# Kernel optimization log

Measured on AMD Instinct MI355X. Metric: run time of the kernel, lower is better.

The kernel has to match this reference:

```python
import jax, jax.numpy as jnp
import numpy as np

HEADS = 8


def setup_inputs() -> dict:
    key = jax.random.key(0)
    ks = jax.random.split(key, 6)
    B, N, D = 4, 2048, 512
    return {
        "x": jax.random.normal(ks[0], (B, N, D), dtype=jnp.float32),
        "pos": jax.random.uniform(ks[1], (B, N, 3), dtype=jnp.float32),
        "qkv_w": jax.random.normal(ks[2], (3 * D, D), dtype=jnp.float32) * 0.02,
        "qkv_b": jax.random.normal(ks[3], (3 * D,), dtype=jnp.float32) * 0.02,
        "out_w": jax.random.normal(ks[4], (D, D), dtype=jnp.float32) * 0.02,
        "out_b": jax.random.normal(ks[5], (D,), dtype=jnp.float32) * 0.02,
    }


def reference(x, pos, qkv_w, qkv_b, out_w, out_b):
    B, N, D = x.shape
    H = HEADS
    Dh = D // H
    scale = D ** (-0.5)  # NOTE: original uses full dim, not head dim

    # QKV projection -> [3, B, H, N, Dh]
    qkv = (x @ qkv_w.T + qkv_b).reshape(B, N, 3, H, Dh).transpose(2, 0, 3, 1, 4)
    q, k, v = qkv[0], qkv[1], qkv[2]

    # partial 3D RoPE on first 6 head dims (3 axis pairs)
    theta = pos * jnp.pi                    # [B, N, 3]
    sin = jnp.sin(theta)[:, None]           # [B, 1, N, 3] broadcasts over heads
    cos = jnp.cos(theta)[:, None]

    def rotate(t):
        x_rot = t[..., :6]
        x1 = x_rot[..., 0::2]               # [B, H, N, 3]
        x2 = x_rot[..., 1::2]
        return jnp.concatenate(
            [x1 * cos - x2 * sin, x1 * sin + x2 * cos, t[..., 6:]], axis=-1
        )

    q = rotate(q)
    k = rotate(k)

    attn = jax.nn.softmax(jnp.einsum("bhqd,bhkd->bhqk", q, k) * scale, axis=-1)
    out = jnp.einsum("bhqk,bhkd->bhqd", attn, v)          # [B, H, N, Dh]
    out = out.transpose(0, 2, 1, 3).reshape(B, N, D)
    return out @ out_w.T + out_b
```

## Files before the change

### kernel.cpp

```cpp
#include <hip/hip_runtime.h>
#include <stdint.h>

typedef __attribute__((ext_vector_type(4))) float f32x4;
typedef __attribute__((ext_vector_type(16))) float f32x16;
typedef __attribute__((ext_vector_type(8))) short bf16x8;
typedef __attribute__((ext_vector_type(4))) unsigned short u16x4;

__device__ __forceinline__ unsigned short f2bf(float f) {
    unsigned int u = __builtin_bit_cast(unsigned int, f);
    u += 0x7fffu + ((u >> 16) & 1u);
    return (unsigned short)(u >> 16);
}
__device__ __forceinline__ float bf2f(unsigned short s) {
    unsigned int u = ((unsigned int)s) << 16;
    return __builtin_bit_cast(float, u);
}
__device__ __forceinline__ float fexp2(float x) {
#if __has_builtin(__builtin_amdgcn_exp2f)
    return __builtin_amdgcn_exp2f(x);
#else
    return exp2f(x);
#endif
}
__device__ __forceinline__ unsigned int cvt_pk_bf16(float lo, float hi) {
    unsigned int r;
    asm("v_cvt_pk_bf16_f32 %0, %1, %2" : "=v"(r) : "v"(lo), "v"(hi));
    return r;
}

__global__ void k_cvt3(const float* __restrict__ x,
                       const float* __restrict__ w1,
                       const float* __restrict__ w2,
                       unsigned short* __restrict__ out) {
    const int C1 = 1048576;
    const int C2 = 196608;
    int i = blockIdx.x * blockDim.x + threadIdx.x;
    f32x4 v;
    if (i < C1)            v = ((const f32x4*)x)[i];
    else if (i < C1 + C2)  v = ((const f32x4*)w1)[i - C1];
    else                   v = ((const f32x4*)w2)[i - C1 - C2];
    u16x4 o;
    o.x = f2bf(v.x); o.y = f2bf(v.y); o.z = f2bf(v.z); o.w = f2bf(v.w);
    ((u16x4*)out)[i] = o;
}

__global__ __launch_bounds__(256, 3)
void k_gemm_qkv(const unsigned short* __restrict__ A,
                const unsigned short* __restrict__ Bm,
                const float* __restrict__ bias,
                const float* __restrict__ pos,
                unsigned short* __restrict__ Qb,
                unsigned short* __restrict__ Kb,
                unsigned short* __restrict__ VT) {
    const float PI = 3.14159265358979323846f;
    const float QS = 0.04419417382415922f * 1.44269504088896341f;
    const int K = 512;
    __shared__ unsigned short As[3][128 * 32];
    __shared__ unsigned short Bs[3][128 * 32];
    const int tid = threadIdx.x;
    const int lane = tid & 63;
    const int w = tid >> 6;
    const int wr = (w >> 1) * 64, wc = (w & 1) * 64;
    const int g = lane >> 4, fr = lane & 15;

    const int bid = blockIdx.x;
    const int xcd = bid & 7, loc = bid >> 3;
    const int rowb = xcd * 8 + (loc & 7);
    const int colb = loc >> 3;

    f32x4 acc[4][4];
#pragma unroll
    for (int i = 0; i < 4; ++i)
#pragma unroll
        for (int j = 0; j < 4; ++j) acc[i][j] = f32x4{0.f, 0.f, 0.f, 0.f};

    const int srow16 = lane >> 2;
    const int schunk = ((lane & 3) ^ (srow16 & 3)) * 8;
    const int sA = w, sB = w + 4;
    const unsigned short* Aseg0 = A + (size_t)(rowb * 128 + sA * 16 + srow16) * K + schunk;
    const unsigned short* Aseg1 = A + (size_t)(rowb * 128 + sB * 16 + srow16) * K + schunk;
    const unsigned short* Bseg0 = Bm + (size_t)(colb * 128 + sA * 16 + srow16) * K + schunk;
    const unsigned short* Bseg1 = Bm + (size_t)(colb * 128 + sB * 16 + srow16) * K + schunk;

    auto stage = [&](int bsel, int k0) {
        char* la = (char*)&As[bsel][0];
        char* lb = (char*)&Bs[bsel][0];
        __builtin_amdgcn_global_load_lds((const __attribute__((address_space(1))) void*)(Aseg0 + k0),
                                         (__attribute__((address_space(3))) void*)(la + sA * 1024), 16, 0, 0);
        __builtin_amdgcn_global_load_lds((const __attribute__((address_space(1))) void*)(Aseg1 + k0),
                                         (__attribute__((address_space(3))) void*)(la + sB * 1024), 16, 0, 0);
        __builtin_amdgcn_global_load_lds((const __attribute__((address_space(1))) void*)(Bseg0 + k0),
                                         (__attribute__((address_space(3))) void*)(lb + sA * 1024), 16, 0, 0);
        __builtin_amdgcn_global_load_lds((const __attribute__((address_space(1))) void*)(Bseg1 + k0),
                                         (__attribute__((address_space(3))) void*)(lb + sB * 1024), 16, 0, 0);
    };
    auto compute = [&](int bsel) {
        bf16x8 af[4], bfv[4];
        const int rc = (g ^ (fr & 3)) * 8;
#pragma unroll
        for (int mi = 0; mi < 4; ++mi)
            af[mi] = *(const bf16x8*)&As[bsel][(wr + mi * 16 + fr) * 32 + rc];
#pragma unroll
        for (int ni = 0; ni < 4; ++ni)
            bfv[ni] = *(const bf16x8*)&Bs[bsel][(wc + ni * 16 + fr) * 32 + rc];
        __builtin_amdgcn_s_setprio(1);
#pragma unroll
        for (int mi = 0; mi < 4; ++mi)
#pragma unroll
            for (int ni = 0; ni < 4; ++ni)
                acc[mi][ni] = __builtin_amdgcn_mfma_f32_16x16x32_bf16(af[mi], bfv[ni], acc[mi][ni], 0, 0, 0);
        __builtin_amdgcn_s_setprio(0);
    };

    const int nt = K >> 5;
    stage(0, 0);
    stage(1, 32);
    int cur = 0;
#pragma unroll 1
    for (int t = 0; t < nt; ++t) {
        if (t < nt - 1) asm volatile("s_waitcnt vmcnt(4)" ::: "memory");
        else            asm volatile("s_waitcnt vmcnt(0)" ::: "memory");
        __builtin_amdgcn_s_barrier();
        compute(cur);
        if (t + 2 < nt) {
            int nxt = cur + 2; if (nxt >= 3) nxt -= 3;
            stage(nxt, (t + 2) << 5);
        }
        cur = (cur + 1 == 3) ? 0 : cur + 1;
    }

    const int jrot = (fr < 3) ? fr : ((fr < 6) ? fr - 3 : 0);
    const int shbase = lane & 48;
#pragma unroll
    for (int mi = 0; mi < 4; ++mi) {
#pragma unroll
        for (int ni = 0; ni < 4; ++ni) {
            int row = rowb * 128 + wr + mi * 16 + g * 4;
            int col = colb * 128 + wc + ni * 16 + fr;
            float bz = bias[col];
            float v[4];
#pragma unroll
            for (int r = 0; r < 4; ++r) v[r] = acc[mi][ni][r] + bz;
            int b = row >> 11, n = row & 2047;
            if (colb < 8) {
                const int isQ = (colb < 4);
                int qcol = isQ ? col : col - 512;
                int h = qcol >> 6, dh = qcol & 63;
                if (ni == 0) {
#pragma unroll
                    for (int r = 0; r < 4; ++r) {
                        float x1 = __shfl(v[r], shbase + 2 * jrot, 64);
                        float x2 = __shfl(v[r], shbase + 2 * jrot + 1, 64);
                        if (fr < 6) {
                            float th = pos[(row + r) * 3 + jrot] * PI;
                            float sn = __sinf(th), cs = __cosf(th);
                            v[r] = (fr < 3) ? (x1 * cs - x2 * sn) : (x1 * sn + x2 * cs);
                        }
                    }
                }
                float qs = isQ ? QS : 1.f;
                unsigned short* dst = isQ ? Qb : Kb;
                size_t rb = (size_t)(b * 8 + h) * 2048 + n;
#pragma unroll
                for (int r = 0; r < 4; ++r)
                    dst[(rb + r) * 64 + dh] = f2bf(v[r] * qs);
            } else {
                int vcol = col - 1024;
                int h = vcol >> 6, dh = vcol & 63;
                int q2 = (n >> 2) & 3;
                int np = n + (q2 == 1 ? 4 : (q2 == 2 ? -4 : 0));
                u16x4 o;
#pragma unroll
                for (int r = 0; r < 4; ++r) o[r] = f2bf(v[r]);
                *(u16x4*)&VT[((size_t)(b * 8 + h) * 64 + dh) * 2048 + np] = o;
            }
        }
    }
}

__global__ __launch_bounds__(256, 3)
void k_gemm_out(const unsigned short* __restrict__ A,
                const unsigned short* __restrict__ Bm,
                const float* __restrict__ bias,
                float* __restrict__ Cout, int M, int N, int K) {
    __shared__ unsigned short As[3][128 * 32];
    __shared__ unsigned short Bs[3][128 * 32];
    const int tid = threadIdx.x;
    const int lane = tid & 63;
    const int w = tid >> 6;
    const int wr = (w >> 1) * 64, wc = (w & 1) * 64;
    const int g = lane >> 4, fr = lane & 15;

    const int bid = blockIdx.x;
    const int xcd = bid & 7, loc = bid >> 3;
    const int rowb = xcd * 8 + (loc & 7);
    const int colb = loc >> 3;

    f32x4 acc[4][4];
#pragma unroll
    for (int i = 0; i < 4; ++i)
#pragma unroll
        for (int j = 0; j < 4; ++j) acc[i][j] = f32x4{0.f, 0.f, 0.f, 0.f};

    const int srow16 = lane >> 2;
    const int schunk = ((lane & 3) ^ (srow16 & 3)) * 8;
    const int sA = w, sB = w + 4;
    const unsigned short* Aseg0 = A + (size_t)(rowb * 128 + sA * 16 + srow16) * K + schunk;
    const unsigned short* Aseg1 = A + (size_t)(rowb * 128 + sB * 16 + srow16) * K + schunk;
    const unsigned short* Bseg0 = Bm + (size_t)(colb * 128 + sA * 16 + srow16) * K + schunk;
    const unsigned short* Bseg1 = Bm + (size_t)(colb * 128 + sB * 16 + srow16) * K + schunk;

    auto stage = [&](int bsel, int k0) {
        char* la = (char*)&As[bsel][0];
        char* lb = (char*)&Bs[bsel][0];
        __builtin_amdgcn_global_load_lds((const __attribute__((address_space(1))) void*)(Aseg0 + k0),
                                         (__attribute__((address_space(3))) void*)(la + sA * 1024), 16, 0, 0);
        __builtin_amdgcn_global_load_lds((const __attribute__((address_space(1))) void*)(Aseg1 + k0),
                                         (__attribute__((address_space(3))) void*)(la + sB * 1024), 16, 0, 0);
        __builtin_amdgcn_global_load_lds((const __attribute__((address_space(1))) void*)(Bseg0 + k0),
                                         (__attribute__((address_space(3))) void*)(lb + sA * 1024), 16, 0, 0);
        __builtin_amdgcn_global_load_lds((const __attribute__((address_space(1))) void*)(Bseg1 + k0),
                                         (__attribute__((address_space(3))) void*)(lb + sB * 1024), 16, 0, 0);
    };
    auto compute = [&](int bsel) {
        bf16x8 af[4], bfv[4];
        const int rc = (g ^ (fr & 3)) * 8;
#pragma unroll
        for (int mi = 0; mi < 4; ++mi)
            af[mi] = *(const bf16x8*)&As[bsel][(wr + mi * 16 + fr) * 32 + rc];
#pragma unroll
        for (int ni = 0; ni < 4; ++ni)
            bfv[ni] = *(const bf16x8*)&Bs[bsel][(wc + ni * 16 + fr) * 32 + rc];
        __builtin_amdgcn_s_setprio(1);
#pragma unroll
        for (int mi = 0; mi < 4; ++mi)
#pragma unroll
            for (int ni = 0; ni < 4; ++ni)
                acc[mi][ni] = __builtin_amdgcn_mfma_f32_16x16x32_bf16(af[mi], bfv[ni], acc[mi][ni], 0, 0, 0);
        __builtin_amdgcn_s_setprio(0);
    };

    const int nt = K >> 5;
    stage(0, 0);
    stage(1, 32);
    int cur = 0;
#pragma unroll 1
    for (int t = 0; t < nt; ++t) {
        if (t < nt - 1) asm volatile("s_waitcnt vmcnt(4)" ::: "memory");
        else            asm volatile("s_waitcnt vmcnt(0)" ::: "memory");
        __builtin_amdgcn_s_barrier();
        compute(cur);
        if (t + 2 < nt) {
            int nxt = cur + 2; if (nxt >= 3) nxt -= 3;
            stage(nxt, (t + 2) << 5);
        }
        cur = (cur + 1 == 3) ? 0 : cur + 1;
    }

#pragma unroll
    for (int mi = 0; mi < 4; ++mi) {
#pragma unroll
        for (int ni = 0; ni < 4; ++ni) {
            int row = rowb * 128 + wr + mi * 16 + g * 4;
            int col = colb * 128 + wc + ni * 16 + fr;
            float bz = bias[col];
#pragma unroll
            for (int r = 0; r < 4; ++r)
                Cout[(size_t)(row + r) * N + col] = acc[mi][ni][r] + bz;
        }
    }
}

__global__ __launch_bounds__(512, 2)
void k_attn(const unsigned short* __restrict__ Qb,
            const unsigned short* __restrict__ Kb,
            const unsigned short* __restrict__ VT,
            unsigned short* __restrict__ Ob) {
    __shared__ unsigned short smem[2][2][2][4096];
    const int tid = threadIdx.x, lane = tid & 63, w = tid >> 6;
    const int wl = w & 3, half = w >> 2;
    const int l31 = lane & 31, hi = lane >> 5;
    const int bid = blockIdx.x;
    const int loc = bid >> 3;
    const int bh = (bid & 7) * 4 + (loc >> 3);
    const int qb = loc & 7;
    const int b = bh >> 3, h = bh & 7;
    const int qr0 = qb * 256 + wl * 64;
    const unsigned short* Q = Qb + (size_t)bh * 2048 * 64;
    const unsigned short* K = Kb + (size_t)bh * 2048 * 64;
    const unsigned short* V = VT + (size_t)bh * 64 * 2048;
    const int thalf = half * 16;

    const int srow8 = lane >> 3;
    const int swc = ((lane & 7) ^ srow8) << 3;
    const int sA = wl, sB = wl + 4;

    bf16x8 bq0[4], bq1[4];
#pragma unroll
    for (int ds = 0; ds < 4; ++ds) {
        bq0[ds] = *(const bf16x8*)&Q[(size_t)(qr0 + l31) * 64 + ds * 16 + hi * 8];
        bq1[ds] = *(const bf16x8*)&Q[(size_t)(qr0 + 32 + l31) * 64 + ds * 16 + hi * 8];
    }

    f32x16 oT00, oT01, oT10, oT11;
#pragma unroll
    for (int i = 0; i < 16; ++i) { oT00[i] = 0.f; oT01[i] = 0.f; oT10[i] = 0.f; oT11[i] = 0.f; }
    float lp0 = 0.f, lp1 = 0.f;

    auto stage = [&](int bsel, int t) {
        const int kv0 = t * 64;
        const unsigned short* k0 = K + (size_t)(kv0 + sA * 8 + srow8) * 64 + swc;
        const unsigned short* k1 = K + (size_t)(kv0 + sB * 8 + srow8) * 64 + swc;
        const unsigned short* v0 = V + (size_t)(sA * 8 + srow8) * 2048 + kv0 + swc;
        const unsigned short* v1 = V + (size_t)(sB * 8 + srow8) * 2048 + kv0 + swc;
        char* dk = (char*)&smem[half][0][bsel][0];
        char* dv = (char*)&smem[half][1][bsel][0];
        __builtin_amdgcn_global_load_lds((const __attribute__((address_space(1))) void*)k0,
                                         (__attribute__((address_space(3))) void*)(dk + sA * 1024), 16, 0, 0);
        __builtin_amdgcn_global_load_lds((const __attribute__((address_space(1))) void*)k1,
                                         (__attribute__((address_space(3))) void*)(dk + sB * 1024), 16, 0, 0);
        __builtin_amdgcn_global_load_lds((const __attribute__((address_space(1))) void*)v0,
                                         (__attribute__((address_space(3))) void*)(dv + sA * 1024), 16, 0, 0);
        __builtin_amdgcn_global_load_lds((const __attribute__((address_space(1))) void*)v1,
                                         (__attribute__((address_space(3))) void*)(dv + sB * 1024), 16, 0, 0);
    };

    auto pack8 = [&](const float* p) -> bf16x8 {
        union { unsigned int u[4]; bf16x8 v; } c;
        c.u[0] = cvt_pk_bf16(p[0], p[1]);
        c.u[1] = cvt_pk_bf16(p[2], p[3]);
        c.u[2] = cvt_pk_bf16(p[4], p[5]);
        c.u[3] = cvt_pk_bf16(p[6], p[7]);
        return c.v;
    };

    auto compute = [&](int bsel) {
        const unsigned short* KsC = &smem[half][0][bsel][0];
        const unsigned short* VtC = &smem[half][1][bsel][0];
        bf16x8 pb0[4], pb1[4];
        {
            f32x16 s0, s1;
#pragma unroll
            for (int i = 0; i < 16; ++i) { s0[i] = 0.f; s1[i] = 0.f; }
            __builtin_amdgcn_s_setprio(1);
#pragma unroll
            for (int ds = 0; ds < 4; ++ds) {
                const int c = ((((ds << 1) | hi) ^ (l31 & 7)) << 3);
                bf16x8 ka0 = *(const bf16x8*)&KsC[l31 * 64 + c];
                bf16x8 ka1 = *(const bf16x8*)&KsC[(32 + l31) * 64 + c];
                s0 = __builtin_amdgcn_mfma_f32_32x32x16_bf16(ka0, bq0[ds], s0, 0, 0, 0);
                s1 = __builtin_amdgcn_mfma_f32_32x32x16_bf16(ka1, bq0[ds], s1, 0, 0, 0);
            }
            __builtin_amdgcn_s_setprio(0);
            float p0[16], p1[16], lsum = 0.f;
#pragma unroll
            for (int r = 0; r < 16; ++r) {
                p0[r] = fexp2(s0[r]);
                p1[r] = fexp2(s1[r]);
                lsum += p0[r] + p1[r];
            }
            lp0 += lsum;
            pb0[0] = pack8(p0); pb0[1] = pack8(p0 + 8);
            pb0[2] = pack8(p1); pb0[3] = pack8(p1 + 8);
        }
        {
            f32x16 s0, s1;
#pragma unroll
            for (int i = 0; i < 16; ++i) { s0[i] = 0.f; s1[i] = 0.f; }
            __builtin_amdgcn_s_setprio(1);
#pragma unroll
            for (int ds = 0; ds < 4; ++ds) {
                const int c = ((((ds << 1) | hi) ^ (l31 & 7)) << 3);
                bf16x8 ka0 = *(const bf16x8*)&KsC[l31 * 64 + c];
                bf16x8 ka1 = *(const bf16x8*)&KsC[(32 + l31) * 64 + c];
                s0 = __builtin_amdgcn_mfma_f32_32x32x16_bf16(ka0, bq1[ds], s0, 0, 0, 0);
                s1 = __builtin_amdgcn_mfma_f32_32x32x16_bf16(ka1, bq1[ds], s1, 0, 0, 0);
            }
            __builtin_amdgcn_s_setprio(0);
            __builtin_amdgcn_s_setprio(1);
#pragma unroll
            for (int kb = 0; kb < 4; ++kb) {
                const int c = ((((kb << 1) | hi) ^ (l31 & 7)) << 3);
                bf16x8 av0 = *(const bf16x8*)&VtC[l31 * 64 + c];
                bf16x8 av1 = *(const bf16x8*)&VtC[(32 + l31) * 64 + c];
                oT00 = __builtin_amdgcn_mfma_f32_32x32x16_bf16(av0, pb0[kb], oT00, 0, 0, 0);
                oT01 = __builtin_amdgcn_mfma_f32_32x32x16_bf16(av1, pb0[kb], oT01, 0, 0, 0);
            }
            __builtin_amdgcn_s_setprio(0);
            float p0[16], p1[16], lsum = 0.f;
#pragma unroll
            for (int r = 0; r < 16; ++r) {
                p0[r] = fexp2(s0[r]);
                p1[r] = fexp2(s1[r]);
                lsum += p0[r] + p1[r];
            }
            lp1 += lsum;
            pb1[0] = pack8(p0); pb1[1] = pack8(p0 + 8);
            pb1[2] = pack8(p1); pb1[3] = pack8(p1 + 8);
        }
        __builtin_amdgcn_s_setprio(1);
#pragma unroll
        for (int kb = 0; kb < 4; ++kb) {
            const int c = ((((kb << 1) | hi) ^ (l31 & 7)) << 3);
            bf16x8 av0 = *(const bf16x8*)&VtC[l31 * 64 + c];
            bf16x8 av1 = *(const bf16x8*)&VtC[(32 + l31) * 64 + c];
            oT10 = __builtin_amdgcn_mfma_f32_32x32x16_bf16(av0, pb1[kb], oT10, 0, 0, 0);
            oT11 = __builtin_amdgcn_mfma_f32_32x32x16_bf16(av1, pb1[kb], oT11, 0, 0, 0);
        }
        __builtin_amdgcn_s_setprio(0);
    };

    stage(0, thalf);
    asm volatile("s_waitcnt vmcnt(0)" ::: "memory");
    __builtin_amdgcn_s_barrier();
    int cur = 0;
#pragma unroll 1
    for (int t = 0; t < 16; ++t) {
        if (t < 15) stage(cur ^ 1, thalf + t + 1);
        compute(cur);
        if (t < 15) {
            asm volatile("s_waitcnt vmcnt(0)" ::: "memory");
            __builtin_amdgcn_s_barrier();
        }
        cur ^= 1;
    }

    float* mrg = (float*)&smem[0][0][0][0];
    float* slot = mrg + (size_t)(wl * 64 + lane) * 33;
#pragma unroll 1
    for (int st = 0; st < 2; ++st) {
        f32x16& a0 = st ? oT10 : oT00;
        f32x16& a1 = st ? oT11 : oT01;
        float lp = st ? lp1 : lp0;
        __syncthreads();
        if (half) {
#pragma unroll
            for (int i = 0; i < 16; ++i) { slot[i] = a0[i]; slot[16 + i] = a1[i]; }
            slot[32] = lp;
        }
        __syncthreads();
        if (!half) {
            float lf = lp + slot[32];
            lf += __shfl_xor(lf, 32, 64);
            float il = 1.f / lf;
            size_t rowbase = (size_t)(b * 2048 + qr0 + st * 32 + l31) * 512 + h * 64;
#pragma unroll
            for (int grp = 0; grp < 4; ++grp) {
                u16x4 o0, o1;
#pragma unroll
                for (int i = 0; i < 4; ++i) {
                    o0[i] = f2bf((a0[grp * 4 + i] + slot[grp * 4 + i]) * il);
                    o1[i] = f2bf((a1[grp * 4 + i] + slot[16 + grp * 4 + i]) * il);
                }
                int dv0 = grp * 8 + 4 * hi;
                *(u16x4*)&Ob[rowbase + dv0] = o0;
                *(u16x4*)&Ob[rowbase + 32 + dv0] = o1;
            }
        }
    }
}

extern "C" void kernel_launch(void* const* d_in, const int* in_sizes, int n_in,
                              void* d_out, int out_size, void* d_ws, size_t ws_size,
                              hipStream_t stream) {
    const float* x     = (const float*)d_in[0];
    const float* pos   = (const float*)d_in[1];
    const float* qkv_w = (const float*)d_in[2];
    const float* qkv_b = (const float*)d_in[3];
    const float* out_w = (const float*)d_in[4];
    const float* out_b = (const float*)d_in[5];
    float* out = (float*)d_out;

    unsigned short* Xb   = (unsigned short*)d_ws;
    unsigned short* W1b  = Xb   + (size_t)8192 * 512;
    unsigned short* W2b  = W1b  + (size_t)1536 * 512;
    unsigned short* Qb   = W2b  + (size_t)512 * 512;
    unsigned short* Kb   = Qb   + (size_t)4194304;
    unsigned short* VTb  = Kb   + (size_t)4194304;
    unsigned short* Ob   = VTb  + (size_t)4194304;

    k_cvt3<<<5120, 256, 0, stream>>>(x, qkv_w, out_w, Xb);
    k_gemm_qkv<<<768, 256, 0, stream>>>(Xb, W1b, qkv_b, pos, Qb, Kb, VTb);
    k_attn<<<256, 512, 0, stream>>>(Qb, Kb, VTb, Ob);
    k_gemm_out<<<256, 256, 0, stream>>>(Ob, W2b, out_b, out, 8192, 512, 512);
}
```

Before: 83.54 us.

## Fuse fp32 X conversion into QKV GEMM and retile output GEMM

Removes the separate fp32-to-bf16 conversion of x. The QKV GEMM now stages fp32 tiles of x into LDS and converts them to bf16 in registers with v_cvt_pk_bf16 before the MFMAs. This saves a full write and re-read of the bf16 copy of x, but doubles the A-tile LDS footprint. Both GEMMs move from a 3-stage to a 2-stage pipeline with a full vmcnt(0) wait each step. The output GEMM uses 128x64 tiles with 512 blocks and 4 waves per SIMD to fill more CUs, at the cost of less reuse per tile.

```diff
diff --git a/kernel.cpp b/kernel.cpp
--- a/kernel.cpp
+++ b/kernel.cpp
@@ -10,10 +10,6 @@
     unsigned int u = __builtin_bit_cast(unsigned int, f);
     u += 0x7fffu + ((u >> 16) & 1u);
     return (unsigned short)(u >> 16);
-}
-__device__ __forceinline__ float bf2f(unsigned short s) {
-    unsigned int u = ((unsigned int)s) << 16;
-    return __builtin_bit_cast(float, u);
 }
 __device__ __forceinline__ float fexp2(float x) {
 #if __has_builtin(__builtin_amdgcn_exp2f)
@@ -28,24 +24,21 @@
     return r;
 }
 
-__global__ void k_cvt3(const float* __restrict__ x,
-                       const float* __restrict__ w1,
+__global__ void k_cvt2(const float* __restrict__ w1,
                        const float* __restrict__ w2,
                        unsigned short* __restrict__ out) {
-    const int C1 = 1048576;
     const int C2 = 196608;
     int i = blockIdx.x * blockDim.x + threadIdx.x;
     f32x4 v;
-    if (i < C1)            v = ((const f32x4*)x)[i];
-    else if (i < C1 + C2)  v = ((const f32x4*)w1)[i - C1];
-    else                   v = ((const f32x4*)w2)[i - C1 - C2];
+    if (i < C2) v = ((const f32x4*)w1)[i];
+    else        v = ((const f32x4*)w2)[i - C2];
     u16x4 o;
     o.x = f2bf(v.x); o.y = f2bf(v.y); o.z = f2bf(v.z); o.w = f2bf(v.w);
     ((u16x4*)out)[i] = o;
 }
 
 __global__ __launch_bounds__(256, 3)
-void k_gemm_qkv(const unsigned short* __restrict__ A,
+void k_gemm_qkv(const float* __restrict__ Xf,
                 const unsigned short* __restrict__ Bm,
                 const float* __restrict__ bias,
                 const float* __restrict__ pos,
@@ -55,8 +48,8 @@
     const float PI = 3.14159265358979323846f;
     const float QS = 0.04419417382415922f * 1.44269504088896341f;
     const int K = 512;
-    __shared__ unsigned short As[3][128 * 32];
-    __shared__ unsigned short Bs[3][128 * 32];
+    __shared__ float Asf[2][128 * 32];
+    __shared__ unsigned short Bs[2][128 * 32];
     const int tid = threadIdx.x;
     const int lane = tid & 63;
     const int w = tid >> 6;
@@ -74,35 +67,47 @@
 #pragma unroll
         for (int j = 0; j < 4; ++j) acc[i][j] = f32x4{0.f, 0.f, 0.f, 0.f};
 
+    const int srow8 = lane >> 3;
+    const int scaf = ((lane & 7) ^ srow8) * 4;
     const int srow16 = lane >> 2;
     const int schunk = ((lane & 3) ^ (srow16 & 3)) * 8;
-    const int sA = w, sB = w + 4;
-    const unsigned short* Aseg0 = A + (size_t)(rowb * 128 + sA * 16 + srow16) * K + schunk;
-    const unsigned short* Aseg1 = A + (size_t)(rowb * 128 + sB * 16 + srow16) * K + schunk;
-    const unsigned short* Bseg0 = Bm + (size_t)(colb * 128 + sA * 16 + srow16) * K + schunk;
-    const unsigned short* Bseg1 = Bm + (size_t)(colb * 128 + sB * 16 + srow16) * K + schunk;
+    const unsigned short* Bseg0 = Bm + (size_t)(colb * 128 + w * 16 + srow16) * K + schunk;
+    const unsigned short* Bseg1 = Bm + (size_t)(colb * 128 + (w + 4) * 16 + srow16) * K + schunk;
 
     auto stage = [&](int bsel, int k0) {
-        char* la = (char*)&As[bsel][0];
+        char* la = (char*)&Asf[bsel][0];
         char* lb = (char*)&Bs[bsel][0];
-        __builtin_amdgcn_global_load_lds((const __attribute__((address_space(1))) void*)(Aseg0 + k0),
-                                         (__attribute__((address_space(3))) void*)(la + sA * 1024), 16, 0, 0);
-        __builtin_amdgcn_global_load_lds((const __attribute__((address_space(1))) void*)(Aseg1 + k0),
-                                         (__attribute__((address_space(3))) void*)(la + sB * 1024), 16, 0, 0);
+#pragma unroll
+        for (int i = 0; i < 4; ++i) {
+            const float* src = Xf + (size_t)(rowb * 128 + (w + 4 * i) * 8 + srow8) * 512 + scaf + k0;
+            __builtin_amdgcn_global_load_lds((const __attribute__((address_space(1))) void*)src,
+                                             (__attribute__((address_space(3))) void*)(la + (w + 4 * i) * 1024), 16, 0, 0);
+        }
         __builtin_amdgcn_global_load_lds((const __attribute__((address_space(1))) void*)(Bseg0 + k0),
-                                         (__attribute__((address_space(3))) void*)(lb + sA * 1024), 16, 0, 0);
+                                         (__attribute__((address_space(3))) void*)(lb + w * 1024), 16, 0, 0);
         __builtin_amdgcn_global_load_lds((const __attribute__((address_space(1))) void*)(Bseg1 + k0),
-                                         (__attribute__((address_space(3))) void*)(lb + sB * 1024), 16, 0, 0);
+                                         (__attribute__((address_space(3))) void*)(lb + (w + 4) * 1024), 16, 0, 0);
     };
     auto compute = [&](int bsel) {
         bf16x8 af[4], bfv[4];
-        const int rc = (g ^ (fr & 3)) * 8;
-#pragma unroll
-        for (int mi = 0; mi < 4; ++mi)
-            af[mi] = *(const bf16x8*)&As[bsel][(wr + mi * 16 + fr) * 32 + rc];
+        const int rcb = (g ^ (fr & 3)) * 8;
+        const int pa0 = ((2 * g) ^ (fr & 7)) * 4;
+        const int pa1 = ((2 * g + 1) ^ (fr & 7)) * 4;
+#pragma unroll
+        for (int mi = 0; mi < 4; ++mi) {
+            int row = wr + mi * 16 + fr;
+            f32x4 lo = *(const f32x4*)&Asf[bsel][row * 32 + pa0];
+            f32x4 hi = *(const f32x4*)&Asf[bsel][row * 32 + pa1];
+            union { unsigned int u[4]; bf16x8 v; } c;
+            c.u[0] = cvt_pk_bf16(lo.x, lo.y);
+            c.u[1] = cvt_pk_bf16(lo.z, lo.w);
+            c.u[2] = cvt_pk_bf16(hi.x, hi.y);
+            c.u[3] = cvt_pk_bf16(hi.z, hi.w);
+            af[mi] = c.v;
+        }
 #pragma unroll
         for (int ni = 0; ni < 4; ++ni)
-            bfv[ni] = *(const bf16x8*)&Bs[bsel][(wc + ni * 16 + fr) * 32 + rc];
+            bfv[ni] = *(const bf16x8*)&Bs[bsel][(wc + ni * 16 + fr) * 32 + rcb];
         __builtin_amdgcn_s_setprio(1);
 #pragma unroll
         for (int mi = 0; mi < 4; ++mi)
@@ -114,19 +119,18 @@
 
     const int nt = K >> 5;
     stage(0, 0);
-    stage(1, 32);
+    asm volatile("s_waitcnt vmcnt(0)" ::: "memory");
+    __builtin_amdgcn_s_barrier();
     int cur = 0;
 #pragma unroll 1
     for (int t = 0; t < nt; ++t) {
-        if (t < nt - 1) asm volatile("s_waitcnt vmcnt(4)" ::: "memory");
-        else            asm volatile("s_waitcnt vmcnt(0)" ::: "memory");
-        __builtin_amdgcn_s_barrier();
+        if (t < nt - 1) stage(cur ^ 1, (t + 1) << 5);
         compute(cur);
-        if (t + 2 < nt) {
-            int nxt = cur + 2; if (nxt >= 3) nxt -= 3;
-            stage(nxt, (t + 2) << 5);
-        }
-        cur = (cur + 1 == 3) ? 0 : cur + 1;
+        if (t < nt - 1) {
+            asm volatile("s_waitcnt vmcnt(0)" ::: "memory");
+            __builtin_amdgcn_s_barrier();
+        }
+        cur ^= 1;
     }
 
     const int jrot = (fr < 3) ? fr : ((fr < 6) ? fr - 3 : 0);
@@ -178,17 +182,18 @@
     }
 }
 
-__global__ __launch_bounds__(256, 3)
+__global__ __launch_bounds__(256, 4)
 void k_gemm_out(const unsigned short* __restrict__ A,
                 const unsigned short* __restrict__ Bm,
                 const float* __restrict__ bias,
-                float* __restrict__ Cout, int M, int N, int K) {
-    __shared__ unsigned short As[3][128 * 32];
-    __shared__ unsigned short Bs[3][128 * 32];
+                float* __restrict__ Cout) {
+    const int K = 512, N = 512;
+    __shared__ unsigned short As[2][128 * 32];
+    __shared__ unsigned short Bs[2][64 * 32];
     const int tid = threadIdx.x;
     const int lane = tid & 63;
     const int w = tid >> 6;
-    const int wr = (w >> 1) * 64, wc = (w & 1) * 64;
+    const int wr = (w >> 1) * 64, wc = (w & 1) * 32;
     const int g = lane >> 4, fr = lane & 15;
 
     const int bid = blockIdx.x;
@@ -196,73 +201,68 @@
     const int rowb = xcd * 8 + (loc & 7);
     const int colb = loc >> 3;
 
-    f32x4 acc[4][4];
+    f32x4 acc[4][2];
 #pragma unroll
     for (int i = 0; i < 4; ++i)
 #pragma unroll
-        for (int j = 0; j < 4; ++j) acc[i][j] = f32x4{0.f, 0.f, 0.f, 0.f};
+        for (int j = 0; j < 2; ++j) acc[i][j] = f32x4{0.f, 0.f, 0.f, 0.f};
 
     const int srow16 = lane >> 2;
     const int schunk = ((lane & 3) ^ (srow16 & 3)) * 8;
-    const int sA = w, sB = w + 4;
-    const unsigned short* Aseg0 = A + (size_t)(rowb * 128 + sA * 16 + srow16) * K + schunk;
-    const unsigned short* Aseg1 = A + (size_t)(rowb * 128 + sB * 16 + srow16) * K + schunk;
-    const unsigned short* Bseg0 = Bm + (size_t)(colb * 128 + sA * 16 + srow16) * K + schunk;
-    const unsigned short* Bseg1 = Bm + (size_t)(colb * 128 + sB * 16 + srow16) * K + schunk;
+    const unsigned short* Aseg0 = A + (size_t)(rowb * 128 + w * 16 + srow16) * K + schunk;
+    const unsigned short* Aseg1 = A + (size_t)(rowb * 128 + (w + 4) * 16 + srow16) * K + schunk;
+    const unsigned short* Bseg  = Bm + (size_t)(colb * 64 + w * 16 + srow16) * K + schunk;
 
     auto stage = [&](int bsel, int k0) {
         char* la = (char*)&As[bsel][0];
         char* lb = (char*)&Bs[bsel][0];
         __builtin_amdgcn_global_load_lds((const __attribute__((address_space(1))) void*)(Aseg0 + k0),
-                                         (__attribute__((address_space(3))) void*)(la + sA * 1024), 16, 0, 0);
+                                         (__attribute__((address_space(3))) void*)(la + w * 1024), 16, 0, 0);
         __builtin_amdgcn_global_load_lds((const __attribute__((address_space(1))) void*)(Aseg1 + k0),
-                                         (__attribute__((address_space(3))) void*)(la + sB * 1024), 16, 0, 0);
-        __builtin_amdgcn_global_load_lds((const __attribute__((address_space(1))) void*)(Bseg0 + k0),
-                                         (__attribute__((address_space(3))) void*)(lb + sA * 1024), 16, 0, 0);
-        __builtin_amdgcn_global_load_lds((const __attribute__((address_space(1))) void*)(Bseg1 + k0),
-                                         (__attribute__((address_space(3))) void*)(lb + sB * 1024), 16, 0, 0);
+                                         (__attribute__((address_space(3))) void*)(la + (w + 4) * 1024), 16, 0, 0);
+        __builtin_amdgcn_global_load_lds((const __attribute__((address_space(1))) void*)(Bseg + k0),
+                                         (__attribute__((address_space(3))) void*)(lb + w * 1024), 16, 0, 0);
     };
     auto compute = [&](int bsel) {
-        bf16x8 af[4], bfv[4];
+        bf16x8 af[4], bfv[2];
         const int rc = (g ^ (fr & 3)) * 8;
 #pragma unroll
         for (int mi = 0; mi < 4; ++mi)
             af[mi] = *(const bf16x8*)&As[bsel][(wr + mi * 16 + fr) * 32 + rc];
 #pragma unroll
-        for (int ni = 0; ni < 4; ++ni)
+        for (int ni = 0; ni < 2; ++ni)
             bfv[ni] = *(const bf16x8*)&Bs[bsel][(wc + ni * 16 + fr) * 32 + rc];
         __builtin_amdgcn_s_setprio(1);
 #pragma unroll
         for (int mi = 0; mi < 4; ++mi)
 #pragma unroll
-            for (int ni = 0; ni < 4; ++ni)
+            for (int ni = 0; ni < 2; ++ni)
                 acc[mi][ni] = __builtin_amdgcn_mfma_f32_16x16x32_bf16(af[mi], bfv[ni], acc[mi][ni], 0, 0, 0);
         __builtin_amdgcn_s_setprio(0);
     };
 
     const int nt = K >> 5;
     stage(0, 0);
-    stage(1, 32);
+    asm volatile("s_waitcnt vmcnt(0)" ::: "memory");
+    __builtin_amdgcn_s_barrier();
     int cur = 0;
 #pragma unroll 1
     for (int t = 0; t < nt; ++t) {
-        if (t < nt - 1) asm volatile("s_waitcnt vmcnt(4)" ::: "memory");
-        else            asm volatile("s_waitcnt vmcnt(0)" ::: "memory");
-        __builtin_amdgcn_s_barrier();
+        if (t < nt - 1) stage(cur ^ 1, (t + 1) << 5);
         compute(cur);
-        if (t + 2 < nt) {
-            int nxt = cur + 2; if (nxt >= 3) nxt -= 3;
-            stage(nxt, (t + 2) << 5);
-        }
-        cur = (cur + 1 == 3) ? 0 : cur + 1;
+        if (t < nt - 1) {
+            asm volatile("s_waitcnt vmcnt(0)" ::: "memory");
+            __builtin_amdgcn_s_barrier();
+        }
+        cur ^= 1;
     }
 
 #pragma unroll
     for (int mi = 0; mi < 4; ++mi) {
 #pragma unroll
-        for (int ni = 0; ni < 4; ++ni) {
+        for (int ni = 0; ni < 2; ++ni) {
             int row = rowb * 128 + wr + mi * 16 + g * 4;
-            int col = colb * 128 + wc + ni * 16 + fr;
+            int col = colb * 64 + wc + ni * 16 + fr;
             float bz = bias[col];
 #pragma unroll
             for (int r = 0; r < 4; ++r)
@@ -471,16 +471,15 @@
     const float* out_b = (const float*)d_in[5];
     float* out = (float*)d_out;
 
-    unsigned short* Xb   = (unsigned short*)d_ws;
-    unsigned short* W1b  = Xb   + (size_t)8192 * 512;
-    unsigned short* W2b  = W1b  + (size_t)1536 * 512;
-    unsigned short* Qb   = W2b  + (size_t)512 * 512;
-    unsigned short* Kb   = Qb   + (size_t)4194304;
-    unsigned short* VTb  = Kb   + (size_t)4194304;
-    unsigned short* Ob   = VTb  + (size_t)4194304;
-
-    k_cvt3<<<5120, 256, 0, stream>>>(x, qkv_w, out_w, Xb);
-    k_gemm_qkv<<<768, 256, 0, stream>>>(Xb, W1b, qkv_b, pos, Qb, Kb, VTb);
+    unsigned short* W1b = (unsigned short*)d_ws;
+    unsigned short* W2b = W1b + (size_t)1536 * 512;
+    unsigned short* Qb  = W2b + (size_t)512 * 512;
+    unsigned short* Kb  = Qb  + (size_t)4194304;
+    unsigned short* VTb = Kb  + (size_t)4194304;
+    unsigned short* Ob  = VTb + (size_t)4194304;
+
+    k_cvt2<<<1024, 256, 0, stream>>>(qkv_w, out_w, W1b);
+    k_gemm_qkv<<<768, 256, 0, stream>>>(x, W1b, qkv_b, pos, Qb, Kb, VTb);
     k_attn<<<256, 512, 0, stream>>>(Qb, Kb, VTb, Ob);
-    k_gemm_out<<<256, 256, 0, stream>>>(Ob, W2b, out_b, out, 8192, 512, 512);
-}
+    k_gemm_out<<<512, 256, 0, stream>>>(Ob, W2b, out_b, out);
+}
```

Result: no change. 83.96 us (+0.5%).
